# Optimization experiments

Measured on AMD Instinct MI355X. Metric: run time of the kernel, lower is better.

Reference implementation:

```python
import jax, jax.numpy as jnp
import numpy as np

S, N, CM, CZ, H, C = 256, 512, 256, 128, 8, 32
EPS = 1e-5


def layer_norm(x, gamma, beta):
    mu = jnp.mean(x, axis=-1, keepdims=True)
    var = jnp.var(x, axis=-1, keepdims=True)
    return (x - mu) * jax.lax.rsqrt(var + EPS) * gamma + beta


def setup_inputs() -> dict:
    key = jax.random.key(0)
    ks = jax.random.split(key, 10)
    sc = lambda fan_in: 1.0 / np.sqrt(fan_in)
    return {
        "msa_rep": jax.random.normal(ks[0], (S, N, CM), dtype=jnp.float32),
        "pair_rep": jax.random.normal(ks[1], (N, N, CZ), dtype=jnp.float32),
        "ln_msa_g": jnp.ones((CM,), jnp.float32),
        "ln_msa_b": jnp.zeros((CM,), jnp.float32),
        "Wv": jax.random.uniform(ks[2], (CM, H * C), jnp.float32, -sc(CM), sc(CM)),
        "bv": jax.random.uniform(ks[3], (H * C,), jnp.float32, -sc(CM), sc(CM)),
        "ln_z_g": jnp.ones((CZ,), jnp.float32),
        "ln_z_b": jnp.zeros((CZ,), jnp.float32),
        "Wb": jax.random.uniform(ks[4], (CZ, H), jnp.float32, -sc(CZ), sc(CZ)),
        "bb": jax.random.uniform(ks[5], (H,), jnp.float32, -sc(CZ), sc(CZ)),
        "Wg": jax.random.uniform(ks[6], (CM, H * C), jnp.float32, -sc(CM), sc(CM)),
        "bg": jax.random.uniform(ks[7], (H * C,), jnp.float32, -sc(CM), sc(CM)),
        "Wp": jax.random.uniform(ks[8], (H * C, CM), jnp.float32, -sc(H * C), sc(H * C)),
    }


def reference(msa_rep, pair_rep, ln_msa_g, ln_msa_b, Wv, bv, ln_z_g, ln_z_b, Wb, bb, Wg, bg, Wp):
    m = layer_norm(msa_rep, ln_msa_g, ln_msa_b)                 # [S,N,CM]
    v = (m @ Wv + bv).reshape(S, N, H, C)                       # [S,N,H,C]
    g = jax.nn.sigmoid(m @ Wg + bg).reshape(S, N, H, C)         # [S,N,H,C]
    b = layer_norm(pair_rep, ln_z_g, ln_z_b) @ Wb + bb          # [N,N,H]
    w = jax.nn.softmax(b, axis=-2)                              # softmax over key residue j
    # o[s,i,h,c] = sum_j w[i,j,h] * v[s,j,h,c]
    o = g * jnp.einsum('ijh,sjhc->sihc', w, v)                  # [S,N,H,C]
    return o.reshape(S, N, H * C) @ Wp                          # [S,N,CM]
```

## Files before the change

kernel.cpp:

```cpp
#include <hip/hip_runtime.h>
#include <hip/hip_bf16.h>
#include <math.h>

#define S 256
#define N 512
#define CM 256
#define CZ 128
#define H 8
#define C 32
#define HC 256

typedef __attribute__((ext_vector_type(8))) short short8v;
typedef __attribute__((ext_vector_type(4))) float f32x4;

#define GLOBAL_LOAD_LDS16(gsrc, ldst)                                          \
  __builtin_amdgcn_global_load_lds(                                            \
      (const __attribute__((address_space(1))) void*)(gsrc),                   \
      (__attribute__((address_space(3))) void*)(ldst), 16, 0, 0)

__global__ __launch_bounds__(256) void k_prep(
    const float* __restrict__ Wv, const float* __restrict__ Wg, const float* __restrict__ Wp,
    __hip_bfloat16* __restrict__ Wcat_t, __hip_bfloat16* __restrict__ Wp_t)
{
  const int k = blockIdx.x;
  const int n = threadIdx.x;
  Wcat_t[(size_t)n * CM + k]        = __float2bfloat16(Wv[(size_t)k * HC + n]);
  Wcat_t[(size_t)(n + HC) * CM + k] = __float2bfloat16(Wg[(size_t)k * HC + n]);
  Wp_t[(size_t)n * CM + k]          = __float2bfloat16(Wp[(size_t)k * CM + n]);
}

__global__ __launch_bounds__(256) void k_ln(
    const float* __restrict__ msa, const float* __restrict__ gamma, const float* __restrict__ beta,
    __hip_bfloat16* __restrict__ mbf)
{
  const int t = threadIdx.x, wav = t >> 6, lane = t & 63;
  const size_t row = (size_t)blockIdx.x * 4 + wav;
  const int k0 = lane * 4;
  const float4 xv = *(const float4*)(msa + row * CM + k0);
  float s  = xv.x + xv.y + xv.z + xv.w;
  float s2 = xv.x * xv.x + xv.y * xv.y + xv.z * xv.z + xv.w * xv.w;
#pragma unroll
  for (int off = 32; off > 0; off >>= 1) {
    s  += __shfl_xor(s, off);
    s2 += __shfl_xor(s2, off);
  }
  const float mu = s * (1.f / CM);
  const float rstd = rsqrtf(s2 * (1.f / CM) - mu * mu + 1e-5f);
  const float4 gm = *(const float4*)(gamma + k0);
  const float4 bt = *(const float4*)(beta + k0);
  union { __hip_bfloat16 b[4]; short4 v; } pk;
  pk.b[0] = __float2bfloat16((xv.x - mu) * rstd * gm.x + bt.x);
  pk.b[1] = __float2bfloat16((xv.y - mu) * rstd * gm.y + bt.y);
  pk.b[2] = __float2bfloat16((xv.z - mu) * rstd * gm.z + bt.z);
  pk.b[3] = __float2bfloat16((xv.w - mu) * rstd * gm.w + bt.w);
  *(short4*)(mbf + row * CM + k0) = pk.v;
}

__global__ __launch_bounds__(512) void k_mm1(
    const __hip_bfloat16* __restrict__ mbf, const __hip_bfloat16* __restrict__ Wcat_t,
    const float* __restrict__ bv, const float* __restrict__ bg,
    __hip_bfloat16* __restrict__ vc, __hip_bfloat16* __restrict__ gb)
{
  __shared__ __hip_bfloat16 Ac[8 * 256 * 8];
  __shared__ __hip_bfloat16 Bc[8 * 128 * 8];
  const int t = threadIdx.x;
  const int wave = t >> 6, lane = t & 63;
  const int wm = wave >> 1, wn = wave & 1;
  const int lr = lane & 15, lq = lane >> 4;
  const int bid = blockIdx.x;
  const int virt = (bid & 7) * 256 + (bid >> 3);
  const int n0 = (virt & 3) * 128;
  const int m0 = (virt >> 2) * 256;
  const bool vhalf = (n0 < HC);

  float bias[4];
#pragma unroll
  for (int ni = 0; ni < 4; ++ni) {
    const int col = n0 + wn * 64 + ni * 16 + lr;
    bias[ni] = vhalf ? bv[col] : bg[col - HC];
  }
  f32x4 acc[4][4];
#pragma unroll
  for (int mi = 0; mi < 4; ++mi)
#pragma unroll
    for (int ni = 0; ni < 4; ++ni) acc[mi][ni] = (f32x4)bias[ni];

  for (int kt = 0; kt < CM / 64; ++kt) {
    __syncthreads();
#pragma unroll
    for (int u = 0; u < 4; ++u) {
      const int cc = wave * 4 + u;
      const int kb = cc & 7, ih = cc >> 3;
      GLOBAL_LOAD_LDS16(mbf + ((size_t)(m0 + ih * 64 + lane)) * CM + kt * 64 + kb * 8,
                        &Ac[(kb * 256 + ih * 64 + lane) * 8]);
    }
#pragma unroll
    for (int u = 0; u < 2; ++u) {
      const int cc = wave * 2 + u;
      const int kb = cc & 7, ih = cc >> 3;
      GLOBAL_LOAD_LDS16(Wcat_t + ((size_t)(n0 + ih * 64 + lane)) * CM + kt * 64 + kb * 8,
                        &Bc[(kb * 128 + ih * 64 + lane) * 8]);
    }
    __syncthreads();
#pragma unroll
    for (int kh = 0; kh < 2; ++kh) {
      const int ldb = lq + kh * 4;
      short8v a[4], b[4];
#pragma unroll
      for (int mi = 0; mi < 4; ++mi)
        a[mi] = *(const short8v*)&Ac[((ldb * 256) + wm * 64 + mi * 16 + lr) * 8];
#pragma unroll
      for (int ni = 0; ni < 4; ++ni)
        b[ni] = *(const short8v*)&Bc[((ldb * 128) + wn * 64 + ni * 16 + lr) * 8];
#pragma unroll
      for (int mi = 0; mi < 4; ++mi)
#pragma unroll
        for (int ni = 0; ni < 4; ++ni)
          acc[mi][ni] = __builtin_amdgcn_mfma_f32_16x16x32_bf16(a[mi], b[ni], acc[mi][ni], 0, 0, 0);
    }
  }

  if (vhalf) {
#pragma unroll
    for (int mi = 0; mi < 4; ++mi) {
      const int rowb = m0 + wm * 64 + mi * 16 + lq * 4;
      const int s = rowb >> 9;
      const int j = rowb & (N - 1);
      const int jb = j >> 3, jlo = (lq & 1) * 4;
#pragma unroll
      for (int ni = 0; ni < 4; ++ni) {
        const int col = n0 + wn * 64 + ni * 16 + lr;
        const int h = col >> 5, c = col & 31;
        union { __hip_bfloat16 b[4]; short4 v; } pk;
#pragma unroll
        for (int r = 0; r < 4; ++r) pk.b[r] = __float2bfloat16(acc[mi][ni][r]);
        *(short4*)(vc + ((size_t)(h * (N / 8) + jb) * (S * C) + s * C + c) * 8 + jlo) = pk.v;
      }
    }
  } else {
#pragma unroll
    for (int mi = 0; mi < 4; ++mi) {
      const int rowb = m0 + wm * 64 + mi * 16 + lq * 4;
#pragma unroll
      for (int ni = 0; ni < 4; ++ni) {
        const int colp = (n0 - HC) + wn * 64 + ni * 16 + lr;
#pragma unroll
        for (int r = 0; r < 4; ++r)
          gb[(size_t)(rowb + r) * HC + colp] =
              __float2bfloat16(1.f / (1.f + __expf(-acc[mi][ni][r])));
      }
    }
  }
}

__global__ __launch_bounds__(256) void k_lnb_sm(
    const float* __restrict__ pair, const float* __restrict__ gamma, const float* __restrict__ beta,
    const float* __restrict__ Wb, __hip_bfloat16* __restrict__ wbh)
{
  __shared__ float slog[H][N];
  const int t = threadIdx.x, wav = t >> 6, lane = t & 63;
  const int q = lane & 15, sub = lane >> 4;
  const int k0 = q * 8;
  const size_t i = blockIdx.x;

  float wreg[8][8];
#pragma unroll
  for (int kk = 0; kk < 8; ++kk) {
    *(float4*)&wreg[kk][0] = *(const float4*)&Wb[(k0 + kk) * H];
    *(float4*)&wreg[kk][4] = *(const float4*)&Wb[(k0 + kk) * H + 4];
  }
  const float4 gm0 = *(const float4*)(gamma + k0);
  const float4 gm1 = *(const float4*)(gamma + k0 + 4);
  const float4 bt0 = *(const float4*)(beta + k0);
  const float4 bt1 = *(const float4*)(beta + k0 + 4);

#pragma unroll 2
  for (int it = 0; it < 32; ++it) {
    const int j = it * 16 + wav * 4 + sub;
    const float* x = pair + (i * N + j) * CZ + k0;
    const float4 x0 = *(const float4*)(x);
    const float4 x1 = *(const float4*)(x + 4);

    float s  = x0.x + x0.y + x0.z + x0.w + x1.x + x1.y + x1.z + x1.w;
    float s2 = x0.x * x0.x + x0.y * x0.y + x0.z * x0.z + x0.w * x0.w
             + x1.x * x1.x + x1.y * x1.y + x1.z * x1.z + x1.w * x1.w;
#pragma unroll
    for (int off = 8; off > 0; off >>= 1) {
      s  += __shfl_xor(s, off);
      s2 += __shfl_xor(s2, off);
    }
    const float mu = s * (1.f / CZ);
    const float rstd = rsqrtf(s2 * (1.f / CZ) - mu * mu + 1e-5f);

    float xn[8];
    xn[0] = (x0.x - mu) * rstd * gm0.x + bt0.x;
    xn[1] = (x0.y - mu) * rstd * gm0.y + bt0.y;
    xn[2] = (x0.z - mu) * rstd * gm0.z + bt0.z;
    xn[3] = (x0.w - mu) * rstd * gm0.w + bt0.w;
    xn[4] = (x1.x - mu) * rstd * gm1.x + bt1.x;
    xn[5] = (x1.y - mu) * rstd * gm1.y + bt1.y;
    xn[6] = (x1.z - mu) * rstd * gm1.z + bt1.z;
    xn[7] = (x1.w - mu) * rstd * gm1.w + bt1.w;

    float acc[8];
#pragma unroll
    for (int h = 0; h < 8; ++h) acc[h] = 0.f;
#pragma unroll
    for (int kk = 0; kk < 8; ++kk)
#pragma unroll
      for (int h = 0; h < 8; ++h) acc[h] += xn[kk] * wreg[kk][h];

#pragma unroll
    for (int h = 0; h < 8; ++h) {
#pragma unroll
      for (int off = 8; off > 0; off >>= 1) acc[h] += __shfl_xor(acc[h], off);
    }
    if (q == 0) {
#pragma unroll
      for (int h = 0; h < 8; ++h) slog[h][j] = acc[h];
    }
  }
  __syncthreads();

#pragma unroll
  for (int hh2 = 0; hh2 < 2; ++hh2) {
    const int hh = wav * 2 + hh2;
    const int j0 = lane * 8;
    const float4 p0 = *(const float4*)&slog[hh][j0];
    const float4 p1 = *(const float4*)&slog[hh][j0 + 4];
    float mx = fmaxf(fmaxf(fmaxf(p0.x, p0.y), fmaxf(p0.z, p0.w)),
                     fmaxf(fmaxf(p1.x, p1.y), fmaxf(p1.z, p1.w)));
#pragma unroll
    for (int off = 32; off > 0; off >>= 1) mx = fmaxf(mx, __shfl_xor(mx, off));
    float e[8];
    e[0] = __expf(p0.x - mx); e[1] = __expf(p0.y - mx);
    e[2] = __expf(p0.z - mx); e[3] = __expf(p0.w - mx);
    e[4] = __expf(p1.x - mx); e[5] = __expf(p1.y - mx);
    e[6] = __expf(p1.z - mx); e[7] = __expf(p1.w - mx);
    float sum = ((e[0] + e[1]) + (e[2] + e[3])) + ((e[4] + e[5]) + (e[6] + e[7]));
#pragma unroll
    for (int off = 32; off > 0; off >>= 1) sum += __shfl_xor(sum, off);
    const float inv = 1.f / sum;
    union { __hip_bfloat16 b[8]; short8v v; } pk;
#pragma unroll
    for (int r = 0; r < 8; ++r) pk.b[r] = __float2bfloat16(e[r] * inv);
    *(short8v*)(wbh + ((size_t)hh * N + i) * N + j0) = pk.v;
  }
}

__global__ __launch_bounds__(512) void k_attn_mfma(
    const __hip_bfloat16* __restrict__ vc, const __hip_bfloat16* __restrict__ wbh,
    __hip_bfloat16* gb)
{
  __shared__ __hip_bfloat16 Ac[8 * 256 * 8];
  __shared__ __hip_bfloat16 Bc[8 * 128 * 8];

  const int t = threadIdx.x;
  const int wave = t >> 6, lane = t & 63;
  const int wm = wave >> 1, wn = wave & 1;
  const int lr = lane & 15, lq = lane >> 4;
  const int bid = blockIdx.x;
  const int virt = (bid & 7) * 128 + (bid >> 3);
  const int h  = virt >> 7;
  const int w_ = virt & 127;
  const int i0 = (w_ >> 6) * 256;
  const int n0 = (w_ & 63) * 128;

  f32x4 acc[4][4];
#pragma unroll
  for (int mi = 0; mi < 4; ++mi)
#pragma unroll
    for (int ni = 0; ni < 4; ++ni) acc[mi][ni] = (f32x4)0.f;

  const __hip_bfloat16* Abase = wbh + ((size_t)h * N + i0) * N;
  const __hip_bfloat16* Bbase = vc + (size_t)h * (N / 8) * (S * C) * 8 + (size_t)n0 * 8;

  for (int kt = 0; kt < N / 64; ++kt) {
    __syncthreads();
#pragma unroll
    for (int u = 0; u < 4; ++u) {
      const int cc = wave * 4 + u;
      const int kb = cc & 7, ih = cc >> 3;
      GLOBAL_LOAD_LDS16(Abase + ((size_t)(ih * 64 + lane)) * N + kt * 64 + kb * 8,
                        &Ac[(kb * 256 + ih * 64 + lane) * 8]);
    }
#pragma unroll
    for (int u = 0; u < 2; ++u) {
      const int cc = wave * 2 + u;
      const int kb = cc & 7, ih = cc >> 3;
      GLOBAL_LOAD_LDS16(Bbase + ((size_t)(kt * 8 + kb) * (S * C) + ih * 64 + lane) * 8,
                        &Bc[(kb * 128 + ih * 64 + lane) * 8]);
    }
    __syncthreads();

#pragma unroll
    for (int kh = 0; kh < 2; ++kh) {
      const int ldb = lq + kh * 4;
      short8v a[4], b[4];
#pragma unroll
      for (int mi = 0; mi < 4; ++mi)
        a[mi] = *(const short8v*)&Ac[((ldb * 256) + wm * 64 + mi * 16 + lr) * 8];
#pragma unroll
      for (int ni = 0; ni < 4; ++ni)
        b[ni] = *(const short8v*)&Bc[((ldb * 128) + wn * 64 + ni * 16 + lr) * 8];
#pragma unroll
      for (int mi = 0; mi < 4; ++mi)
#pragma unroll
        for (int ni = 0; ni < 4; ++ni)
          acc[mi][ni] = __builtin_amdgcn_mfma_f32_16x16x32_bf16(a[mi], b[ni], acc[mi][ni], 0, 0, 0);
    }
  }

#pragma unroll
  for (int mi = 0; mi < 4; ++mi)
#pragma unroll
    for (int ni = 0; ni < 4; ++ni) {
      const int n = n0 + wn * 64 + ni * 16 + lr;
      const int sidx = n >> 5, c = n & 31;
#pragma unroll
      for (int r = 0; r < 4; ++r) {
        const int i = i0 + wm * 64 + mi * 16 + lq * 4 + r;
        const size_t idx = (((size_t)sidx * N + i) << 8) + h * C + c;
        const float gv = __bfloat162float(gb[idx]);
        gb[idx] = __float2bfloat16(gv * acc[mi][ni][r]);
      }
    }
}

__global__ __launch_bounds__(512) void k_out_mfma(
    const __hip_bfloat16* __restrict__ ogb, const __hip_bfloat16* __restrict__ Wp_t,
    float* __restrict__ out)
{
  __shared__ __hip_bfloat16 Ac[8 * 256 * 8];
  __shared__ __hip_bfloat16 Bc[8 * 128 * 8];
  const int t = threadIdx.x;
  const int wave = t >> 6, lane = t & 63;
  const int wm = wave >> 1, wn = wave & 1;
  const int lr = lane & 15, lq = lane >> 4;
  const int bid = blockIdx.x;
  const int virt = (bid & 7) * 128 + (bid >> 3);
  const int n0 = (virt & 1) * 128;
  const int m0 = (virt >> 1) * 256;

  f32x4 acc[4][4];
#pragma unroll
  for (int mi = 0; mi < 4; ++mi)
#pragma unroll
    for (int ni = 0; ni < 4; ++ni) acc[mi][ni] = (f32x4)0.f;

  for (int kt = 0; kt < CM / 64; ++kt) {
    __syncthreads();
#pragma unroll
    for (int u = 0; u < 4; ++u) {
      const int cc = wave * 4 + u;
      const int kb = cc & 7, ih = cc >> 3;
      GLOBAL_LOAD_LDS16(ogb + ((size_t)(m0 + ih * 64 + lane)) * CM + kt * 64 + kb * 8,
                        &Ac[(kb * 256 + ih * 64 + lane) * 8]);
    }
#pragma unroll
    for (int u = 0; u < 2; ++u) {
      const int cc = wave * 2 + u;
      const int kb = cc & 7, ih = cc >> 3;
      GLOBAL_LOAD_LDS16(Wp_t + ((size_t)(n0 + ih * 64 + lane)) * CM + kt * 64 + kb * 8,
                        &Bc[(kb * 128 + ih * 64 + lane) * 8]);
    }
    __syncthreads();
#pragma unroll
    for (int kh = 0; kh < 2; ++kh) {
      const int ldb = lq + kh * 4;
      short8v a[4], b[4];
#pragma unroll
      for (int mi = 0; mi < 4; ++mi)
        a[mi] = *(const short8v*)&Ac[((ldb * 256) + wm * 64 + mi * 16 + lr) * 8];
#pragma unroll
      for (int ni = 0; ni < 4; ++ni)
        b[ni] = *(const short8v*)&Bc[((ldb * 128) + wn * 64 + ni * 16 + lr) * 8];
#pragma unroll
      for (int mi = 0; mi < 4; ++mi)
#pragma unroll
        for (int ni = 0; ni < 4; ++ni)
          acc[mi][ni] = __builtin_amdgcn_mfma_f32_16x16x32_bf16(a[mi], b[ni], acc[mi][ni], 0, 0, 0);
    }
  }

#pragma unroll
  for (int mi = 0; mi < 4; ++mi) {
    const int rowb = m0 + wm * 64 + mi * 16 + lq * 4;
#pragma unroll
    for (int ni = 0; ni < 4; ++ni) {
      const int col = n0 + wn * 64 + ni * 16 + lr;
#pragma unroll
      for (int r = 0; r < 4; ++r)
        out[(size_t)(rowb + r) * CM + col] = acc[mi][ni][r];
    }
  }
}

extern "C" void kernel_launch(void* const* d_in, const int* in_sizes, int n_in,
                              void* d_out, int out_size, void* d_ws, size_t ws_size,
                              hipStream_t stream)
{
  const float* msa      = (const float*)d_in[0];
  const float* pair     = (const float*)d_in[1];
  const float* ln_msa_g = (const float*)d_in[2];
  const float* ln_msa_b = (const float*)d_in[3];
  const float* Wv       = (const float*)d_in[4];
  const float* bv       = (const float*)d_in[5];
  const float* ln_z_g   = (const float*)d_in[6];
  const float* ln_z_b   = (const float*)d_in[7];
  const float* Wb       = (const float*)d_in[8];
  const float* bb       = (const float*)d_in[9];
  const float* Wg       = (const float*)d_in[10];
  const float* bg       = (const float*)d_in[11];
  const float* Wp       = (const float*)d_in[12];
  float* out = (float*)d_out;
  (void)bb;

  char* w = (char*)d_ws;
  __hip_bfloat16* vc     = (__hip_bfloat16*)(w);
  __hip_bfloat16* mbf    = (__hip_bfloat16*)(w + 67108864);
  __hip_bfloat16* gb     = (__hip_bfloat16*)(w + 134217728);
  __hip_bfloat16* wbh    = (__hip_bfloat16*)(w + 209715200);
  __hip_bfloat16* Wcat_t = (__hip_bfloat16*)(w + 213909504);
  __hip_bfloat16* Wp_t   = (__hip_bfloat16*)(w + 214171648);

  k_prep<<<256, 256, 0, stream>>>(Wv, Wg, Wp, Wcat_t, Wp_t);
  k_ln<<<S * N / 4, 256, 0, stream>>>(msa, ln_msa_g, ln_msa_b, mbf);
  k_mm1<<<2048, 512, 0, stream>>>(mbf, Wcat_t, bv, bg, vc, gb);
  k_lnb_sm<<<N, 256, 0, stream>>>(pair, ln_z_g, ln_z_b, Wb, wbh);
  k_attn_mfma<<<1024, 512, 0, stream>>>(vc, wbh, gb);
  k_out_mfma<<<1024, 512, 0, stream>>>(gb, Wp_t, out);
}
```

Before: 327.1 us.

## Pipeline LDS staging in split K-halves across three MFMA GEMM kernels

```diff
diff --git a/kernel.cpp b/kernel.cpp
--- a/kernel.cpp
+++ b/kernel.cpp
@@ -85,39 +85,66 @@
 #pragma unroll
     for (int ni = 0; ni < 4; ++ni) acc[mi][ni] = (f32x4)bias[ni];
 
-  for (int kt = 0; kt < CM / 64; ++kt) {
-    __syncthreads();
-#pragma unroll
-    for (int u = 0; u < 4; ++u) {
-      const int cc = wave * 4 + u;
-      const int kb = cc & 7, ih = cc >> 3;
+  auto stage_lo = [&](int kt) {
+#pragma unroll
+    for (int u = 0; u < 2; ++u) {
+      const int cL = wave * 2 + u;
+      const int kb = cL & 3, ih = cL >> 2;
       GLOBAL_LOAD_LDS16(mbf + ((size_t)(m0 + ih * 64 + lane)) * CM + kt * 64 + kb * 8,
                         &Ac[(kb * 256 + ih * 64 + lane) * 8]);
     }
-#pragma unroll
-    for (int u = 0; u < 2; ++u) {
-      const int cc = wave * 2 + u;
-      const int kb = cc & 7, ih = cc >> 3;
+    {
+      const int kb = wave & 3, ih = wave >> 2;
       GLOBAL_LOAD_LDS16(Wcat_t + ((size_t)(n0 + ih * 64 + lane)) * CM + kt * 64 + kb * 8,
                         &Bc[(kb * 128 + ih * 64 + lane) * 8]);
     }
-    __syncthreads();
-#pragma unroll
-    for (int kh = 0; kh < 2; ++kh) {
-      const int ldb = lq + kh * 4;
-      short8v a[4], b[4];
-#pragma unroll
-      for (int mi = 0; mi < 4; ++mi)
-        a[mi] = *(const short8v*)&Ac[((ldb * 256) + wm * 64 + mi * 16 + lr) * 8];
+  };
+  auto stage_hi = [&](int kt) {
+#pragma unroll
+    for (int u = 0; u < 2; ++u) {
+      const int cL = wave * 2 + u;
+      const int kb = (cL & 3) + 4, ih = cL >> 2;
+      GLOBAL_LOAD_LDS16(mbf + ((size_t)(m0 + ih * 64 + lane)) * CM + kt * 64 + kb * 8,
+                        &Ac[(kb * 256 + ih * 64 + lane) * 8]);
+    }
+    {
+      const int kb = (wave & 3) + 4, ih = wave >> 2;
+      GLOBAL_LOAD_LDS16(Wcat_t + ((size_t)(n0 + ih * 64 + lane)) * CM + kt * 64 + kb * 8,
+                        &Bc[(kb * 128 + ih * 64 + lane) * 8]);
+    }
+  };
+  auto compute = [&](int kh) {
+    const int ldb = lq + kh * 4;
+    short8v a[4], b[4];
+#pragma unroll
+    for (int mi = 0; mi < 4; ++mi)
+      a[mi] = *(const short8v*)&Ac[((ldb * 256) + wm * 64 + mi * 16 + lr) * 8];
+#pragma unroll
+    for (int ni = 0; ni < 4; ++ni)
+      b[ni] = *(const short8v*)&Bc[((ldb * 128) + wn * 64 + ni * 16 + lr) * 8];
+#pragma unroll
+    for (int mi = 0; mi < 4; ++mi)
 #pragma unroll
       for (int ni = 0; ni < 4; ++ni)
-        b[ni] = *(const short8v*)&Bc[((ldb * 128) + wn * 64 + ni * 16 + lr) * 8];
-#pragma unroll
-      for (int mi = 0; mi < 4; ++mi)
-#pragma unroll
-        for (int ni = 0; ni < 4; ++ni)
-          acc[mi][ni] = __builtin_amdgcn_mfma_f32_16x16x32_bf16(a[mi], b[ni], acc[mi][ni], 0, 0, 0);
-    }
+        acc[mi][ni] = __builtin_amdgcn_mfma_f32_16x16x32_bf16(a[mi], b[ni], acc[mi][ni], 0, 0, 0);
+  };
+
+  const int NT = CM / 64;
+  stage_lo(0);
+  stage_hi(0);
+  asm volatile("s_waitcnt vmcnt(3)" ::: "memory");
+  __builtin_amdgcn_s_barrier();
+  for (int kt = 0; kt < NT; ++kt) {
+    compute(0);
+    asm volatile("s_waitcnt vmcnt(0) lgkmcnt(0)" ::: "memory");
+    __builtin_amdgcn_s_barrier();
+    if (kt + 1 < NT) stage_lo(kt + 1);
+    compute(1);
+    asm volatile("s_waitcnt lgkmcnt(0)" ::: "memory");
+    __builtin_amdgcn_s_barrier();
+    if (kt + 1 < NT) stage_hi(kt + 1);
+    asm volatile("s_waitcnt vmcnt(3)" ::: "memory");
+    __builtin_amdgcn_s_barrier();
   }
 
   if (vhalf) {
@@ -275,56 +302,84 @@
   const __hip_bfloat16* Abase = wbh + ((size_t)h * N + i0) * N;
   const __hip_bfloat16* Bbase = vc + (size_t)h * (N / 8) * (S * C) * 8 + (size_t)n0 * 8;
 
-  for (int kt = 0; kt < N / 64; ++kt) {
-    __syncthreads();
-#pragma unroll
-    for (int u = 0; u < 4; ++u) {
-      const int cc = wave * 4 + u;
-      const int kb = cc & 7, ih = cc >> 3;
+  auto stage_lo = [&](int kt) {
+#pragma unroll
+    for (int u = 0; u < 2; ++u) {
+      const int cL = wave * 2 + u;
+      const int kb = cL & 3, ih = cL >> 2;
       GLOBAL_LOAD_LDS16(Abase + ((size_t)(ih * 64 + lane)) * N + kt * 64 + kb * 8,
                         &Ac[(kb * 256 + ih * 64 + lane) * 8]);
     }
-#pragma unroll
-    for (int u = 0; u < 2; ++u) {
-      const int cc = wave * 2 + u;
-      const int kb = cc & 7, ih = cc >> 3;
+    {
+      const int kb = wave & 3, ih = wave >> 2;
       GLOBAL_LOAD_LDS16(Bbase + ((size_t)(kt * 8 + kb) * (S * C) + ih * 64 + lane) * 8,
                         &Bc[(kb * 128 + ih * 64 + lane) * 8]);
     }
-    __syncthreads();
-
-#pragma unroll
-    for (int kh = 0; kh < 2; ++kh) {
-      const int ldb = lq + kh * 4;
-      short8v a[4], b[4];
-#pragma unroll
-      for (int mi = 0; mi < 4; ++mi)
-        a[mi] = *(const short8v*)&Ac[((ldb * 256) + wm * 64 + mi * 16 + lr) * 8];
+  };
+  auto stage_hi = [&](int kt) {
+#pragma unroll
+    for (int u = 0; u < 2; ++u) {
+      const int cL = wave * 2 + u;
+      const int kb = (cL & 3) + 4, ih = cL >> 2;
+      GLOBAL_LOAD_LDS16(Abase + ((size_t)(ih * 64 + lane)) * N + kt * 64 + kb * 8,
+                        &Ac[(kb * 256 + ih * 64 + lane) * 8]);
+    }
+    {
+      const int kb = (wave & 3) + 4, ih = wave >> 2;
+      GLOBAL_LOAD_LDS16(Bbase + ((size_t)(kt * 8 + kb) * (S * C) + ih * 64 + lane) * 8,
+                        &Bc[(kb * 128 + ih * 64 + lane) * 8]);
+    }
+  };
+  auto compute = [&](int kh) {
+    const int ldb = lq + kh * 4;
+    short8v a[4], b[4];
+#pragma unroll
+    for (int mi = 0; mi < 4; ++mi)
+      a[mi] = *(const short8v*)&Ac[((ldb * 256) + wm * 64 + mi * 16 + lr) * 8];
+#pragma unroll
+    for (int ni = 0; ni < 4; ++ni)
+      b[ni] = *(const short8v*)&Bc[((ldb * 128) + wn * 64 + ni * 16 + lr) * 8];
+#pragma unroll
+    for (int mi = 0; mi < 4; ++mi)
 #pragma unroll
       for (int ni = 0; ni < 4; ++ni)
-        b[ni] = *(const short8v*)&Bc[((ldb * 128) + wn * 64 + ni * 16 + lr) * 8];
-#pragma unroll
-      for (int mi = 0; mi < 4; ++mi)
-#pragma unroll
-        for (int ni = 0; ni < 4; ++ni)
-          acc[mi][ni] = __builtin_amdgcn_mfma_f32_16x16x32_bf16(a[mi], b[ni], acc[mi][ni], 0, 0, 0);
-    }
-  }
-
-#pragma unroll
-  for (int mi = 0; mi < 4; ++mi)
+        acc[mi][ni] = __builtin_amdgcn_mfma_f32_16x16x32_bf16(b[ni], a[mi], acc[mi][ni], 0, 0, 0);
+  };
+
+  const int NT = N / 64;
+  stage_lo(0);
+  stage_hi(0);
+  asm volatile("s_waitcnt vmcnt(3)" ::: "memory");
+  __builtin_amdgcn_s_barrier();
+  for (int kt = 0; kt < NT; ++kt) {
+    compute(0);
+    asm volatile("s_waitcnt vmcnt(0) lgkmcnt(0)" ::: "memory");
+    __builtin_amdgcn_s_barrier();
+    if (kt + 1 < NT) stage_lo(kt + 1);
+    compute(1);
+    asm volatile("s_waitcnt lgkmcnt(0)" ::: "memory");
+    __builtin_amdgcn_s_barrier();
+    if (kt + 1 < NT) stage_hi(kt + 1);
+    asm volatile("s_waitcnt vmcnt(3)" ::: "memory");
+    __builtin_amdgcn_s_barrier();
+  }
+
+#pragma unroll
+  for (int mi = 0; mi < 4; ++mi) {
+    const int i = i0 + wm * 64 + mi * 16 + lr;
 #pragma unroll
     for (int ni = 0; ni < 4; ++ni) {
-      const int n = n0 + wn * 64 + ni * 16 + lr;
-      const int sidx = n >> 5, c = n & 31;
-#pragma unroll
-      for (int r = 0; r < 4; ++r) {
-        const int i = i0 + wm * 64 + mi * 16 + lq * 4 + r;
-        const size_t idx = (((size_t)sidx * N + i) << 8) + h * C + c;
-        const float gv = __bfloat162float(gb[idx]);
-        gb[idx] = __float2bfloat16(gv * acc[mi][ni][r]);
-      }
-    }
+      const int nb = n0 + wn * 64 + ni * 16 + lq * 4;
+      const int sidx = nb >> 5, c = nb & 31;
+      __hip_bfloat16* gp = gb + (((size_t)sidx * N + i) << 8) + h * C + c;
+      union { __hip_bfloat16 b[4]; short4 v; } gl, st;
+      gl.v = *(const short4*)gp;
+#pragma unroll
+      for (int r = 0; r < 4; ++r)
+        st.b[r] = __float2bfloat16(__bfloat162float(gl.b[r]) * acc[mi][ni][r]);
+      *(short4*)gp = st.v;
+    }
+  }
 }
 
 __global__ __launch_bounds__(512) void k_out_mfma(
@@ -348,39 +403,66 @@
 #pragma unroll
     for (int ni = 0; ni < 4; ++ni) acc[mi][ni] = (f32x4)0.f;
 
-  for (int kt = 0; kt < CM / 64; ++kt) {
-    __syncthreads();
-#pragma unroll
-    for (int u = 0; u < 4; ++u) {
-      const int cc = wave * 4 + u;
-      const int kb = cc & 7, ih = cc >> 3;
+  auto stage_lo = [&](int kt) {
+#pragma unroll
+    for (int u = 0; u < 2; ++u) {
+      const int cL = wave * 2 + u;
+      const int kb = cL & 3, ih = cL >> 2;
       GLOBAL_LOAD_LDS16(ogb + ((size_t)(m0 + ih * 64 + lane)) * CM + kt * 64 + kb * 8,
                         &Ac[(kb * 256 + ih * 64 + lane) * 8]);
     }
-#pragma unroll
-    for (int u = 0; u < 2; ++u) {
-      const int cc = wave * 2 + u;
-      const int kb = cc & 7, ih = cc >> 3;
+    {
+      const int kb = wave & 3, ih = wave >> 2;
       GLOBAL_LOAD_LDS16(Wp_t + ((size_t)(n0 + ih * 64 + lane)) * CM + kt * 64 + kb * 8,
                         &Bc[(kb * 128 + ih * 64 + lane) * 8]);
     }
-    __syncthreads();
-#pragma unroll
-    for (int kh = 0; kh < 2; ++kh) {
-      const int ldb = lq + kh * 4;
-      short8v a[4], b[4];
-#pragma unroll
-      for (int mi = 0; mi < 4; ++mi)
-        a[mi] = *(const short8v*)&Ac[((ldb * 256) + wm * 64 + mi * 16 + lr) * 8];
+  };
+  auto stage_hi = [&](int kt) {
+#pragma unroll
+    for (int u = 0; u < 2; ++u) {
+      const int cL = wave * 2 + u;
+      const int kb = (cL & 3) + 4, ih = cL >> 2;
+      GLOBAL_LOAD_LDS16(ogb + ((size_t)(m0 + ih * 64 + lane)) * CM + kt * 64 + kb * 8,
+                        &Ac[(kb * 256 + ih * 64 + lane) * 8]);
+    }
+    {
+      const int kb = (wave & 3) + 4, ih = wave >> 2;
+      GLOBAL_LOAD_LDS16(Wp_t + ((size_t)(n0 + ih * 64 + lane)) * CM + kt * 64 + kb * 8,
+                        &Bc[(kb * 128 + ih * 64 + lane) * 8]);
+    }
+  };
+  auto compute = [&](int kh) {
+    const int ldb = lq + kh * 4;
+    short8v a[4], b[4];
+#pragma unroll
+    for (int mi = 0; mi < 4; ++mi)
+      a[mi] = *(const short8v*)&Ac[((ldb * 256) + wm * 64 + mi * 16 + lr) * 8];
+#pragma unroll
+    for (int ni = 0; ni < 4; ++ni)
+      b[ni] = *(const short8v*)&Bc[((ldb * 128) + wn * 64 + ni * 16 + lr) * 8];
+#pragma unroll
+    for (int mi = 0; mi < 4; ++mi)
 #pragma unroll
       for (int ni = 0; ni < 4; ++ni)
-        b[ni] = *(const short8v*)&Bc[((ldb * 128) + wn * 64 + ni * 16 + lr) * 8];
-#pragma unroll
-      for (int mi = 0; mi < 4; ++mi)
-#pragma unroll
-        for (int ni = 0; ni < 4; ++ni)
-          acc[mi][ni] = __builtin_amdgcn_mfma_f32_16x16x32_bf16(a[mi], b[ni], acc[mi][ni], 0, 0, 0);
-    }
+        acc[mi][ni] = __builtin_amdgcn_mfma_f32_16x16x32_bf16(a[mi], b[ni], acc[mi][ni], 0, 0, 0);
+  };
+
+  const int NT = CM / 64;
+  stage_lo(0);
+  stage_hi(0);
+  asm volatile("s_waitcnt vmcnt(3)" ::: "memory");
+  __builtin_amdgcn_s_barrier();
+  for (int kt = 0; kt < NT; ++kt) {
+    compute(0);
+    asm volatile("s_waitcnt vmcnt(0) lgkmcnt(0)" ::: "memory");
+    __builtin_amdgcn_s_barrier();
+    if (kt + 1 < NT) stage_lo(kt + 1);
+    compute(1);
+    asm volatile("s_waitcnt lgkmcnt(0)" ::: "memory");
+    __builtin_amdgcn_s_barrier();
+    if (kt + 1 < NT) stage_hi(kt + 1);
+    asm volatile("s_waitcnt vmcnt(3)" ::: "memory");
+    __builtin_amdgcn_s_barrier();
   }
 
 #pragma unroll
```

Result: slower. 348.1 us (+6.4%).

## Double-buffer LDS tiles in all three MFMA GEMM kernels with BK=32

Applied to the files above, without the earlier changes.

```diff
diff --git a/kernel.cpp b/kernel.cpp
--- a/kernel.cpp
+++ b/kernel.cpp
@@ -61,8 +61,8 @@
     const float* __restrict__ bv, const float* __restrict__ bg,
     __hip_bfloat16* __restrict__ vc, __hip_bfloat16* __restrict__ gb)
 {
-  __shared__ __hip_bfloat16 Ac[8 * 256 * 8];
-  __shared__ __hip_bfloat16 Bc[8 * 128 * 8];
+  __shared__ __hip_bfloat16 Ac[2][4 * 256 * 8];
+  __shared__ __hip_bfloat16 Bc[2][4 * 128 * 8];
   const int t = threadIdx.x;
   const int wave = t >> 6, lane = t & 63;
   const int wm = wave >> 1, wn = wave & 1;
@@ -85,39 +85,44 @@
 #pragma unroll
     for (int ni = 0; ni < 4; ++ni) acc[mi][ni] = (f32x4)bias[ni];
 
-  for (int kt = 0; kt < CM / 64; ++kt) {
-    __syncthreads();
-#pragma unroll
-    for (int u = 0; u < 4; ++u) {
-      const int cc = wave * 4 + u;
-      const int kb = cc & 7, ih = cc >> 3;
-      GLOBAL_LOAD_LDS16(mbf + ((size_t)(m0 + ih * 64 + lane)) * CM + kt * 64 + kb * 8,
-                        &Ac[(kb * 256 + ih * 64 + lane) * 8]);
-    }
+  auto stage = [&](int p, int kt) {
 #pragma unroll
     for (int u = 0; u < 2; ++u) {
       const int cc = wave * 2 + u;
-      const int kb = cc & 7, ih = cc >> 3;
-      GLOBAL_LOAD_LDS16(Wcat_t + ((size_t)(n0 + ih * 64 + lane)) * CM + kt * 64 + kb * 8,
-                        &Bc[(kb * 128 + ih * 64 + lane) * 8]);
-    }
+      const int kb = cc & 3, ih = cc >> 2;
+      GLOBAL_LOAD_LDS16(mbf + ((size_t)(m0 + ih * 64 + lane)) * CM + kt * 32 + kb * 8,
+                        &Ac[p][(kb * 256 + ih * 64 + lane) * 8]);
+    }
+    {
+      const int kb = wave & 3, ih = wave >> 2;
+      GLOBAL_LOAD_LDS16(Wcat_t + ((size_t)(n0 + ih * 64 + lane)) * CM + kt * 32 + kb * 8,
+                        &Bc[p][(kb * 128 + ih * 64 + lane) * 8]);
+    }
+  };
+  auto compute = [&](int p) {
+    short8v a[4], b[4];
+#pragma unroll
+    for (int mi = 0; mi < 4; ++mi)
+      a[mi] = *(const short8v*)&Ac[p][((lq * 256) + wm * 64 + mi * 16 + lr) * 8];
+#pragma unroll
+    for (int ni = 0; ni < 4; ++ni)
+      b[ni] = *(const short8v*)&Bc[p][((lq * 128) + wn * 64 + ni * 16 + lr) * 8];
+#pragma unroll
+    for (int mi = 0; mi < 4; ++mi)
+#pragma unroll
+      for (int ni = 0; ni < 4; ++ni)
+        acc[mi][ni] = __builtin_amdgcn_mfma_f32_16x16x32_bf16(a[mi], b[ni], acc[mi][ni], 0, 0, 0);
+  };
+
+  const int NT = CM / 32;
+  stage(0, 0);
+  __syncthreads();
+  int cur = 0;
+  for (int kt = 0; kt < NT; ++kt) {
+    if (kt + 1 < NT) stage(cur ^ 1, kt + 1);
+    compute(cur);
     __syncthreads();
-#pragma unroll
-    for (int kh = 0; kh < 2; ++kh) {
-      const int ldb = lq + kh * 4;
-      short8v a[4], b[4];
-#pragma unroll
-      for (int mi = 0; mi < 4; ++mi)
-        a[mi] = *(const short8v*)&Ac[((ldb * 256) + wm * 64 + mi * 16 + lr) * 8];
-#pragma unroll
-      for (int ni = 0; ni < 4; ++ni)
-        b[ni] = *(const short8v*)&Bc[((ldb * 128) + wn * 64 + ni * 16 + lr) * 8];
-#pragma unroll
-      for (int mi = 0; mi < 4; ++mi)
-#pragma unroll
-        for (int ni = 0; ni < 4; ++ni)
-          acc[mi][ni] = __builtin_amdgcn_mfma_f32_16x16x32_bf16(a[mi], b[ni], acc[mi][ni], 0, 0, 0);
-    }
+    cur ^= 1;
   }
 
   if (vhalf) {
@@ -252,8 +257,8 @@
     const __hip_bfloat16* __restrict__ vc, const __hip_bfloat16* __restrict__ wbh,
     __hip_bfloat16* gb)
 {
-  __shared__ __hip_bfloat16 Ac[8 * 256 * 8];
-  __shared__ __hip_bfloat16 Bc[8 * 128 * 8];
+  __shared__ __hip_bfloat16 Ac[2][4 * 256 * 8];
+  __shared__ __hip_bfloat16 Bc[2][4 * 128 * 8];
 
   const int t = threadIdx.x;
   const int wave = t >> 6, lane = t & 63;
@@ -275,40 +280,44 @@
   const __hip_bfloat16* Abase = wbh + ((size_t)h * N + i0) * N;
   const __hip_bfloat16* Bbase = vc + (size_t)h * (N / 8) * (S * C) * 8 + (size_t)n0 * 8;
 
-  for (int kt = 0; kt < N / 64; ++kt) {
-    __syncthreads();
-#pragma unroll
-    for (int u = 0; u < 4; ++u) {
-      const int cc = wave * 4 + u;
-      const int kb = cc & 7, ih = cc >> 3;
-      GLOBAL_LOAD_LDS16(Abase + ((size_t)(ih * 64 + lane)) * N + kt * 64 + kb * 8,
-                        &Ac[(kb * 256 + ih * 64 + lane) * 8]);
-    }
+  auto stage = [&](int p, int kt) {
 #pragma unroll
     for (int u = 0; u < 2; ++u) {
       const int cc = wave * 2 + u;
-      const int kb = cc & 7, ih = cc >> 3;
-      GLOBAL_LOAD_LDS16(Bbase + ((size_t)(kt * 8 + kb) * (S * C) + ih * 64 + lane) * 8,
-                        &Bc[(kb * 128 + ih * 64 + lane) * 8]);
-    }
+      const int kb = cc & 3, ih = cc >> 2;
+      GLOBAL_LOAD_LDS16(Abase + ((size_t)(ih * 64 + lane)) * N + kt * 32 + kb * 8,
+                        &Ac[p][(kb * 256 + ih * 64 + lane) * 8]);
+    }
+    {
+      const int kb = wave & 3, ih = wave >> 2;
+      GLOBAL_LOAD_LDS16(Bbase + ((size_t)(kt * 4 + kb) * (S * C) + ih * 64 + lane) * 8,
+                        &Bc[p][(kb * 128 + ih * 64 + lane) * 8]);
+    }
+  };
+  auto compute = [&](int p) {
+    short8v a[4], b[4];
+#pragma unroll
+    for (int mi = 0; mi < 4; ++mi)
+      a[mi] = *(const short8v*)&Ac[p][((lq * 256) + wm * 64 + mi * 16 + lr) * 8];
+#pragma unroll
+    for (int ni = 0; ni < 4; ++ni)
+      b[ni] = *(const short8v*)&Bc[p][((lq * 128) + wn * 64 + ni * 16 + lr) * 8];
+#pragma unroll
+    for (int mi = 0; mi < 4; ++mi)
+#pragma unroll
+      for (int ni = 0; ni < 4; ++ni)
+        acc[mi][ni] = __builtin_amdgcn_mfma_f32_16x16x32_bf16(a[mi], b[ni], acc[mi][ni], 0, 0, 0);
+  };
+
+  const int NT = N / 32;
+  stage(0, 0);
+  __syncthreads();
+  int cur = 0;
+  for (int kt = 0; kt < NT; ++kt) {
+    if (kt + 1 < NT) stage(cur ^ 1, kt + 1);
+    compute(cur);
     __syncthreads();
-
-#pragma unroll
-    for (int kh = 0; kh < 2; ++kh) {
-      const int ldb = lq + kh * 4;
-      short8v a[4], b[4];
-#pragma unroll
-      for (int mi = 0; mi < 4; ++mi)
-        a[mi] = *(const short8v*)&Ac[((ldb * 256) + wm * 64 + mi * 16 + lr) * 8];
-#pragma unroll
-      for (int ni = 0; ni < 4; ++ni)
-        b[ni] = *(const short8v*)&Bc[((ldb * 128) + wn * 64 + ni * 16 + lr) * 8];
-#pragma unroll
-      for (int mi = 0; mi < 4; ++mi)
-#pragma unroll
-        for (int ni = 0; ni < 4; ++ni)
-          acc[mi][ni] = __builtin_amdgcn_mfma_f32_16x16x32_bf16(a[mi], b[ni], acc[mi][ni], 0, 0, 0);
-    }
+    cur ^= 1;
   }
 
 #pragma unroll
@@ -331,8 +340,8 @@
     const __hip_bfloat16* __restrict__ ogb, const __hip_bfloat16* __restrict__ Wp_t,
     float* __restrict__ out)
 {
-  __shared__ __hip_bfloat16 Ac[8 * 256 * 8];
-  __shared__ __hip_bfloat16 Bc[8 * 128 * 8];
+  __shared__ __hip_bfloat16 Ac[2][4 * 256 * 8];
+  __shared__ __hip_bfloat16 Bc[2][4 * 128 * 8];
   const int t = threadIdx.x;
   const int wave = t >> 6, lane = t & 63;
   const int wm = wave >> 1, wn = wave & 1;
@@ -348,39 +357,44 @@
 #pragma unroll
     for (int ni = 0; ni < 4; ++ni) acc[mi][ni] = (f32x4)0.f;
 
-  for (int kt = 0; kt < CM / 64; ++kt) {
-    __syncthreads();
-#pragma unroll
-    for (int u = 0; u < 4; ++u) {
-      const int cc = wave * 4 + u;
-      const int kb = cc & 7, ih = cc >> 3;
-      GLOBAL_LOAD_LDS16(ogb + ((size_t)(m0 + ih * 64 + lane)) * CM + kt * 64 + kb * 8,
-                        &Ac[(kb * 256 + ih * 64 + lane) * 8]);
-    }
+  auto stage = [&](int p, int kt) {
 #pragma unroll
     for (int u = 0; u < 2; ++u) {
       const int cc = wave * 2 + u;
-      const int kb = cc & 7, ih = cc >> 3;
-      GLOBAL_LOAD_LDS16(Wp_t + ((size_t)(n0 + ih * 64 + lane)) * CM + kt * 64 + kb * 8,
-                        &Bc[(kb * 128 + ih * 64 + lane) * 8]);
-    }
+      const int kb = cc & 3, ih = cc >> 2;
+      GLOBAL_LOAD_LDS16(ogb + ((size_t)(m0 + ih * 64 + lane)) * CM + kt * 32 + kb * 8,
+                        &Ac[p][(kb * 256 + ih * 64 + lane) * 8]);
+    }
+    {
+      const int kb = wave & 3, ih = wave >> 2;
+      GLOBAL_LOAD_LDS16(Wp_t + ((size_t)(n0 + ih * 64 + lane)) * CM + kt * 32 + kb * 8,
+                        &Bc[p][(kb * 128 + ih * 64 + lane) * 8]);
+    }
+  };
+  auto compute = [&](int p) {
+    short8v a[4], b[4];
+#pragma unroll
+    for (int mi = 0; mi < 4; ++mi)
+      a[mi] = *(const short8v*)&Ac[p][((lq * 256) + wm * 64 + mi * 16 + lr) * 8];
+#pragma unroll
+    for (int ni = 0; ni < 4; ++ni)
+      b[ni] = *(const short8v*)&Bc[p][((lq * 128) + wn * 64 + ni * 16 + lr) * 8];
+#pragma unroll
+    for (int mi = 0; mi < 4; ++mi)
+#pragma unroll
+      for (int ni = 0; ni < 4; ++ni)
+        acc[mi][ni] = __builtin_amdgcn_mfma_f32_16x16x32_bf16(a[mi], b[ni], acc[mi][ni], 0, 0, 0);
+  };
+
+  const int NT = CM / 32;
+  stage(0, 0);
+  __syncthreads();
+  int cur = 0;
+  for (int kt = 0; kt < NT; ++kt) {
+    if (kt + 1 < NT) stage(cur ^ 1, kt + 1);
+    compute(cur);
     __syncthreads();
-#pragma unroll
-    for (int kh = 0; kh < 2; ++kh) {
-      const int ldb = lq + kh * 4;
-      short8v a[4], b[4];
-#pragma unroll
-      for (int mi = 0; mi < 4; ++mi)
-        a[mi] = *(const short8v*)&Ac[((ldb * 256) + wm * 64 + mi * 16 + lr) * 8];
-#pragma unroll
-      for (int ni = 0; ni < 4; ++ni)
-        b[ni] = *(const short8v*)&Bc[((ldb * 128) + wn * 64 + ni * 16 + lr) * 8];
-#pragma unroll
-      for (int mi = 0; mi < 4; ++mi)
-#pragma unroll
-        for (int ni = 0; ni < 4; ++ni)
-          acc[mi][ni] = __builtin_amdgcn_mfma_f32_16x16x32_bf16(a[mi], b[ni], acc[mi][ni], 0, 0, 0);
-    }
+    cur ^= 1;
   }
 
 #pragma unroll
```

After: 365.3 us. +11.7%, slower.

## Double-buffer LDS tiles in attention MFMA kernel with async prefetch

Applied to the files above, without the earlier changes.

```diff
diff --git a/kernel.cpp b/kernel.cpp
--- a/kernel.cpp
+++ b/kernel.cpp
@@ -252,8 +252,8 @@
     const __hip_bfloat16* __restrict__ vc, const __hip_bfloat16* __restrict__ wbh,
     __hip_bfloat16* gb)
 {
-  __shared__ __hip_bfloat16 Ac[8 * 256 * 8];
-  __shared__ __hip_bfloat16 Bc[8 * 128 * 8];
+  __shared__ __hip_bfloat16 Ac[2][4 * 256 * 8];
+  __shared__ __hip_bfloat16 Bc[2][4 * 128 * 8];
 
   const int t = threadIdx.x;
   const int wave = t >> 6, lane = t & 63;
@@ -275,41 +275,51 @@
   const __hip_bfloat16* Abase = wbh + ((size_t)h * N + i0) * N;
   const __hip_bfloat16* Bbase = vc + (size_t)h * (N / 8) * (S * C) * 8 + (size_t)n0 * 8;
 
-  for (int kt = 0; kt < N / 64; ++kt) {
-    __syncthreads();
-#pragma unroll
-    for (int u = 0; u < 4; ++u) {
-      const int cc = wave * 4 + u;
-      const int kb = cc & 7, ih = cc >> 3;
-      GLOBAL_LOAD_LDS16(Abase + ((size_t)(ih * 64 + lane)) * N + kt * 64 + kb * 8,
-                        &Ac[(kb * 256 + ih * 64 + lane) * 8]);
-    }
+  auto stage = [&](int p, int kt) {
 #pragma unroll
     for (int u = 0; u < 2; ++u) {
       const int cc = wave * 2 + u;
-      const int kb = cc & 7, ih = cc >> 3;
-      GLOBAL_LOAD_LDS16(Bbase + ((size_t)(kt * 8 + kb) * (S * C) + ih * 64 + lane) * 8,
-                        &Bc[(kb * 128 + ih * 64 + lane) * 8]);
-    }
-    __syncthreads();
-
-#pragma unroll
-    for (int kh = 0; kh < 2; ++kh) {
-      const int ldb = lq + kh * 4;
-      short8v a[4], b[4];
-#pragma unroll
-      for (int mi = 0; mi < 4; ++mi)
-        a[mi] = *(const short8v*)&Ac[((ldb * 256) + wm * 64 + mi * 16 + lr) * 8];
+      const int kb = cc & 3, ih = cc >> 2;
+      GLOBAL_LOAD_LDS16(Abase + ((size_t)(ih * 64 + lane)) * N + kt * 32 + kb * 8,
+                        &Ac[p][(kb * 256 + ih * 64 + lane) * 8]);
+    }
+    {
+      const int kb = wave & 3, ih = wave >> 2;
+      GLOBAL_LOAD_LDS16(Bbase + ((size_t)(kt * 4 + kb) * (S * C) + ih * 64 + lane) * 8,
+                        &Bc[p][(kb * 128 + ih * 64 + lane) * 8]);
+    }
+  };
+  auto compute = [&](int p) {
+    short8v a[4], b[4];
+#pragma unroll
+    for (int mi = 0; mi < 4; ++mi)
+      a[mi] = *(const short8v*)&Ac[p][((lq * 256) + wm * 64 + mi * 16 + lr) * 8];
+#pragma unroll
+    for (int ni = 0; ni < 4; ++ni)
+      b[ni] = *(const short8v*)&Bc[p][((lq * 128) + wn * 64 + ni * 16 + lr) * 8];
+#pragma unroll
+    for (int mi = 0; mi < 4; ++mi)
 #pragma unroll
       for (int ni = 0; ni < 4; ++ni)
-        b[ni] = *(const short8v*)&Bc[((ldb * 128) + wn * 64 + ni * 16 + lr) * 8];
-#pragma unroll
-      for (int mi = 0; mi < 4; ++mi)
-#pragma unroll
-        for (int ni = 0; ni < 4; ++ni)
-          acc[mi][ni] = __builtin_amdgcn_mfma_f32_16x16x32_bf16(a[mi], b[ni], acc[mi][ni], 0, 0, 0);
-    }
-  }
+        acc[mi][ni] = __builtin_amdgcn_mfma_f32_16x16x32_bf16(a[mi], b[ni], acc[mi][ni], 0, 0, 0);
+  };
+
+  const int NT = N / 32;
+  stage(0, 0);
+  stage(1, 1);
+  for (int kt = 0; kt < NT - 1; ++kt) {
+    asm volatile("s_waitcnt vmcnt(3)" ::: "memory");
+    __builtin_amdgcn_s_barrier();
+    __builtin_amdgcn_sched_barrier(0);
+    compute(kt & 1);
+    __builtin_amdgcn_s_barrier();
+    __builtin_amdgcn_sched_barrier(0);
+    if (kt + 2 < NT) stage(kt & 1, kt + 2);
+  }
+  asm volatile("s_waitcnt vmcnt(0)" ::: "memory");
+  __builtin_amdgcn_s_barrier();
+  __builtin_amdgcn_sched_barrier(0);
+  compute((NT - 1) & 1);
 
 #pragma unroll
   for (int mi = 0; mi < 4; ++mi)
```

New measurement: 341.4 us. 4.4% more time.
